# Kernel optimization log

Hardware: AMD Instinct MI355X
Metric: run time of the kernel (lower is better)

Reference implementation:

```python
import jax, jax.numpy as jnp
import numpy as np


def _demosaic_kernels():
    kgrb = 1/8 * np.array([[0,0,-1,0,0],[0,0,2,0,0],[-1,2,4,2,-1],[0,0,2,0,0],[0,0,-1,0,0]], dtype=np.float32)
    krbg0 = 1/8 * np.array([[0,0,0.5,0,0],[0,-1,0,-1,0],[-1,4,5,4,-1],[0,-1,0,-1,0],[0,0,0.5,0,0]], dtype=np.float32)
    krbg1 = krbg0.T
    krbbr = 1/8 * np.array([[0,0,-1.5,0,0],[0,2,0,2,0],[-1.5,0,6,0,-1.5],[0,2,0,2,0],[0,0,-1.5,0,0]], dtype=np.float32)
    return jnp.asarray(np.stack([kgrb, krbg0, krbg1, krbbr], 0)[:, None, :, :])  # (4,1,5,5)


def setup_inputs() -> dict:
    key = jax.random.key(0)
    x = jax.random.uniform(key, (4, 1, 2048, 2048), dtype=jnp.float32)  # RGGB bayer mosaic
    k = _demosaic_kernels()
    return {"x": x, "k": k}


def reference(x, k):
    # reflect-pad by 2 on H and W, then fixed 4-filter 5x5 conv
    xp = jnp.pad(x, ((0, 0), (0, 0), (2, 2), (2, 2)), mode="reflect")
    cfa = jax.lax.conv_general_dilated(
        xp, k, window_strides=(1, 1), padding="VALID",
        dimension_numbers=("NCHW", "OIHW", "NCHW"))  # (N,4,H,W)
    out = jnp.tile(x, (1, 3, 1, 1))  # (N,3,H,W)
    # green at R and B sites
    out = out.at[:, 1, 0::2, 0::2].set(cfa[:, 0, 0::2, 0::2])
    out = out.at[:, 1, 1::2, 1::2].set(cfa[:, 0, 1::2, 1::2])
    # red at G/B sites
    out = out.at[:, 0, 0::2, 1::2].set(cfa[:, 1, 0::2, 1::2])
    out = out.at[:, 0, 1::2, 0::2].set(cfa[:, 2, 1::2, 0::2])
    out = out.at[:, 0, 1::2, 1::2].set(cfa[:, 3, 1::2, 1::2])
    # blue at G/R sites
    out = out.at[:, 2, 0::2, 1::2].set(cfa[:, 2, 0::2, 1::2])
    out = out.at[:, 2, 1::2, 0::2].set(cfa[:, 1, 1::2, 0::2])
    out = out.at[:, 2, 0::2, 0::2].set(cfa[:, 3, 0::2, 0::2])
    return jnp.clip(out, 0.0, 1.0)
```

## Files before the change

kernel.cpp:

```cpp
#include <hip/hip_runtime.h>

#define IMG_H 2048
#define IMG_W 2048
#define NIMG 4

__device__ __forceinline__ int refl(int i, int n) {
    i = (i < 0) ? -i : i;
    return (i >= n) ? (2 * n - 2 - i) : i;
}

__device__ __forceinline__ float clamp01(float v) {
    return fminf(fmaxf(v, 0.0f), 1.0f);
}

__device__ __forceinline__ void px_rgb(
    float x0,
    float xl, float xr, float xll, float xrr,
    float xu, float xd, float xuu, float xdd,
    float dul, float dur, float ddl, float ddr,
    int pr, int pc,
    float& R, float& G, float& B)
{
    float h1 = xl + xr, v1 = xu + xd;
    float h2 = xll + xrr, v2 = xuu + xdd;
    float diag = dul + dur + ddl + ddr;
    float cfa0 = 0.125f * (4.0f * x0 + 2.0f * (h1 + v1) - (h2 + v2));
    float cfa1 = 0.125f * (5.0f * x0 + 4.0f * h1 - h2 + 0.5f * v2 - diag);
    float cfa2 = 0.125f * (5.0f * x0 + 4.0f * v1 - v2 + 0.5f * h2 - diag);
    float cfa3 = 0.125f * (6.0f * x0 + 2.0f * diag - 1.5f * (h2 + v2));

    if (pr == 0) {
        if (pc == 0) { R = x0;   G = cfa0; B = cfa3; }
        else         { R = cfa1; G = x0;   B = cfa2; }
    } else {
        if (pc == 0) { R = cfa2; G = x0;   B = cfa1; }
        else         { R = cfa3; G = cfa0; B = x0;   }
    }
    R = clamp01(R); G = clamp01(G); B = clamp01(B);
}

__global__ __launch_bounds__(256) void demosaic_kernel(
    const float* __restrict__ x, float* __restrict__ out)
{
    const int QW = IMG_W / 4;
    int idx = blockIdx.x * blockDim.x + threadIdx.x;
    int c4   = idx & (QW - 1);
    int rest = idx >> 9;
    int r = rest & (IMG_H - 1);
    int n = rest >> 11;
    int c = c4 * 4;

    const float* p = x + (size_t)n * IMG_H * IMG_W;
    int pr = r & 1;
    float R[4], G[4], B[4];

    bool interior = (r >= 2) && (r <= IMG_H - 3) && (c >= 4) && (c <= IMG_W - 8);
    if (interior) {
        const float* pm2 = p + (size_t)(r - 2) * IMG_W + c;
        const float* pm1 = p + (size_t)(r - 1) * IMG_W + c;
        const float* p0  = p + (size_t)(r    ) * IMG_W + c;
        const float* pp1 = p + (size_t)(r + 1) * IMG_W + c;
        const float* pp2 = p + (size_t)(r + 2) * IMG_W + c;

        float w0[8], wm1[6], wp1[6], wm2[4], wp2[4];
        #pragma unroll
        for (int i = 0; i < 8; i++) w0[i] = p0[i - 2];
        #pragma unroll
        for (int i = 0; i < 6; i++) { wm1[i] = pm1[i - 1]; wp1[i] = pp1[i - 1]; }
        #pragma unroll
        for (int i = 0; i < 4; i++) { wm2[i] = pm2[i]; wp2[i] = pp2[i]; }

        #pragma unroll
        for (int j = 0; j < 4; j++) {
            px_rgb(w0[j + 2],
                   w0[j + 1], w0[j + 3], w0[j], w0[j + 4],
                   wm1[j + 1], wp1[j + 1], wm2[j], wp2[j],
                   wm1[j], wm1[j + 2], wp1[j], wp1[j + 2],
                   pr, j & 1,
                   R[j], G[j], B[j]);
        }
    } else {
        int rm1 = refl(r - 1, IMG_H), rm2 = refl(r - 2, IMG_H);
        int rp1 = refl(r + 1, IMG_H), rp2 = refl(r + 2, IMG_H);
        const float* p0r  = p + (size_t)r   * IMG_W;
        const float* pm1r = p + (size_t)rm1 * IMG_W;
        const float* pm2r = p + (size_t)rm2 * IMG_W;
        const float* pp1r = p + (size_t)rp1 * IMG_W;
        const float* pp2r = p + (size_t)rp2 * IMG_W;
        #pragma unroll
        for (int j = 0; j < 4; j++) {
            int cc  = c + j;
            int cm1 = refl(cc - 1, IMG_W), cm2 = refl(cc - 2, IMG_W);
            int cp1 = refl(cc + 1, IMG_W), cp2 = refl(cc + 2, IMG_W);
            px_rgb(p0r[cc],
                   p0r[cm1], p0r[cp1], p0r[cm2], p0r[cp2],
                   pm1r[cc], pp1r[cc], pm2r[cc], pp2r[cc],
                   pm1r[cm1], pm1r[cp1], pp1r[cm1], pp1r[cp1],
                   pr, cc & 1,
                   R[j], G[j], B[j]);
        }
    }

    const size_t plane = (size_t)IMG_H * IMG_W;
    size_t ob = (size_t)n * 3 * plane + (size_t)r * IMG_W + c;
    *(float4*)(out + ob)             = make_float4(R[0], R[1], R[2], R[3]);
    *(float4*)(out + ob + plane)     = make_float4(G[0], G[1], G[2], G[3]);
    *(float4*)(out + ob + 2 * plane) = make_float4(B[0], B[1], B[2], B[3]);
}

extern "C" void kernel_launch(void* const* d_in, const int* in_sizes, int n_in,
                              void* d_out, int out_size, void* d_ws, size_t ws_size,
                              hipStream_t stream) {
    const float* x = (const float*)d_in[0];
    float* out = (float*)d_out;
    const int total = NIMG * IMG_H * (IMG_W / 4);
    dim3 block(256);
    dim3 grid(total / 256);
    demosaic_kernel<<<grid, block, 0, stream>>>(x, out);
}
```

Before: 272.9 us.

## Process two rows per thread with aligned float4 neighborhood loads

Each thread now computes a 2x4 pixel block covering both Bayer row parities instead of a 1x4 strip, and the grid is halved to match. The 6-row stencil window is fetched as aligned float4 loads and shared between the two output rows, which cuts redundant neighbor reads and removes runtime parity branching. The cost is more registers per thread and half as many threads in flight. The kernel is memory-bound, so the gain depends mostly on fewer load instructions, since cache traffic was already mostly reused.

```diff
diff --git a/kernel.cpp b/kernel.cpp
--- a/kernel.cpp
+++ b/kernel.cpp
@@ -42,70 +42,93 @@
 __global__ __launch_bounds__(256) void demosaic_kernel(
     const float* __restrict__ x, float* __restrict__ out)
 {
-    const int QW = IMG_W / 4;
     int idx = blockIdx.x * blockDim.x + threadIdx.x;
-    int c4   = idx & (QW - 1);
+    int c4   = idx & 511;
     int rest = idx >> 9;
-    int r = rest & (IMG_H - 1);
-    int n = rest >> 11;
-    int c = c4 * 4;
+    int rp   = rest & 1023;
+    int n    = rest >> 10;
+    int r = rp << 1;
+    int c = c4 << 2;
 
     const float* p = x + (size_t)n * IMG_H * IMG_W;
-    int pr = r & 1;
-    float R[4], G[4], B[4];
+    const size_t plane = (size_t)IMG_H * IMG_W;
+    size_t ob = (size_t)n * 3 * plane + (size_t)r * IMG_W + c;
 
-    bool interior = (r >= 2) && (r <= IMG_H - 3) && (c >= 4) && (c <= IMG_W - 8);
+    bool interior = (r >= 2) && (r <= IMG_H - 4) && (c >= 4) && (c <= IMG_W - 8);
     if (interior) {
-        const float* pm2 = p + (size_t)(r - 2) * IMG_W + c;
-        const float* pm1 = p + (size_t)(r - 1) * IMG_W + c;
-        const float* p0  = p + (size_t)(r    ) * IMG_W + c;
-        const float* pp1 = p + (size_t)(r + 1) * IMG_W + c;
-        const float* pp2 = p + (size_t)(r + 2) * IMG_W + c;
+        const float* b = p + (size_t)r * IMG_W + c;
+        float4 m2  = *(const float4*)(b - 2 * IMG_W);
+        float4 m1l = *(const float4*)(b - IMG_W - 4);
+        float4 m1c = *(const float4*)(b - IMG_W);
+        float4 m1r = *(const float4*)(b - IMG_W + 4);
+        float4 z0l = *(const float4*)(b - 4);
+        float4 z0c = *(const float4*)(b);
+        float4 z0r = *(const float4*)(b + 4);
+        float4 z1l = *(const float4*)(b + IMG_W - 4);
+        float4 z1c = *(const float4*)(b + IMG_W);
+        float4 z1r = *(const float4*)(b + IMG_W + 4);
+        float4 z2l = *(const float4*)(b + 2 * IMG_W - 4);
+        float4 z2c = *(const float4*)(b + 2 * IMG_W);
+        float4 z2r = *(const float4*)(b + 2 * IMG_W + 4);
+        float4 p3  = *(const float4*)(b + 3 * IMG_W);
 
-        float w0[8], wm1[6], wp1[6], wm2[4], wp2[4];
-        #pragma unroll
-        for (int i = 0; i < 8; i++) w0[i] = p0[i - 2];
-        #pragma unroll
-        for (int i = 0; i < 6; i++) { wm1[i] = pm1[i - 1]; wp1[i] = pp1[i - 1]; }
-        #pragma unroll
-        for (int i = 0; i < 4; i++) { wm2[i] = pm2[i]; wp2[i] = pp2[i]; }
+        float wm2[4] = {m2.x, m2.y, m2.z, m2.w};
+        float wm1[6] = {m1l.w, m1c.x, m1c.y, m1c.z, m1c.w, m1r.x};
+        float w0[8]  = {z0l.z, z0l.w, z0c.x, z0c.y, z0c.z, z0c.w, z0r.x, z0r.y};
+        float w1[8]  = {z1l.z, z1l.w, z1c.x, z1c.y, z1c.z, z1c.w, z1r.x, z1r.y};
+        float w2[6]  = {z2l.w, z2c.x, z2c.y, z2c.z, z2c.w, z2r.x};
+        float w3[4]  = {p3.x, p3.y, p3.z, p3.w};
 
+        float R0[4], G0[4], B0[4], R1[4], G1[4], B1[4];
         #pragma unroll
         for (int j = 0; j < 4; j++) {
             px_rgb(w0[j + 2],
                    w0[j + 1], w0[j + 3], w0[j], w0[j + 4],
-                   wm1[j + 1], wp1[j + 1], wm2[j], wp2[j],
-                   wm1[j], wm1[j + 2], wp1[j], wp1[j + 2],
-                   pr, j & 1,
-                   R[j], G[j], B[j]);
+                   wm1[j + 1], w1[j + 2], wm2[j], w2[j + 1],
+                   wm1[j], wm1[j + 2], w1[j + 1], w1[j + 3],
+                   0, j & 1, R0[j], G0[j], B0[j]);
+            px_rgb(w1[j + 2],
+                   w1[j + 1], w1[j + 3], w1[j], w1[j + 4],
+                   w0[j + 2], w2[j + 1], wm1[j + 1], w3[j],
+                   w0[j + 1], w0[j + 3], w2[j], w2[j + 2],
+                   1, j & 1, R1[j], G1[j], B1[j]);
         }
+
+        *(float4*)(out + ob)                     = make_float4(R0[0], R0[1], R0[2], R0[3]);
+        *(float4*)(out + ob + plane)             = make_float4(G0[0], G0[1], G0[2], G0[3]);
+        *(float4*)(out + ob + 2 * plane)         = make_float4(B0[0], B0[1], B0[2], B0[3]);
+        *(float4*)(out + ob + IMG_W)             = make_float4(R1[0], R1[1], R1[2], R1[3]);
+        *(float4*)(out + ob + IMG_W + plane)     = make_float4(G1[0], G1[1], G1[2], G1[3]);
+        *(float4*)(out + ob + IMG_W + 2 * plane) = make_float4(B1[0], B1[1], B1[2], B1[3]);
     } else {
-        int rm1 = refl(r - 1, IMG_H), rm2 = refl(r - 2, IMG_H);
-        int rp1 = refl(r + 1, IMG_H), rp2 = refl(r + 2, IMG_H);
-        const float* p0r  = p + (size_t)r   * IMG_W;
-        const float* pm1r = p + (size_t)rm1 * IMG_W;
-        const float* pm2r = p + (size_t)rm2 * IMG_W;
-        const float* pp1r = p + (size_t)rp1 * IMG_W;
-        const float* pp2r = p + (size_t)rp2 * IMG_W;
         #pragma unroll
-        for (int j = 0; j < 4; j++) {
-            int cc  = c + j;
-            int cm1 = refl(cc - 1, IMG_W), cm2 = refl(cc - 2, IMG_W);
-            int cp1 = refl(cc + 1, IMG_W), cp2 = refl(cc + 2, IMG_W);
-            px_rgb(p0r[cc],
-                   p0r[cm1], p0r[cp1], p0r[cm2], p0r[cp2],
-                   pm1r[cc], pp1r[cc], pm2r[cc], pp2r[cc],
-                   pm1r[cm1], pm1r[cp1], pp1r[cm1], pp1r[cp1],
-                   pr, cc & 1,
-                   R[j], G[j], B[j]);
+        for (int i = 0; i < 2; i++) {
+            int rr = r + i;
+            int rm1 = refl(rr - 1, IMG_H), rm2 = refl(rr - 2, IMG_H);
+            int rp1 = refl(rr + 1, IMG_H), rp2 = refl(rr + 2, IMG_H);
+            const float* p0r  = p + (size_t)rr  * IMG_W;
+            const float* pm1r = p + (size_t)rm1 * IMG_W;
+            const float* pm2r = p + (size_t)rm2 * IMG_W;
+            const float* pp1r = p + (size_t)rp1 * IMG_W;
+            const float* pp2r = p + (size_t)rp2 * IMG_W;
+            #pragma unroll
+            for (int j = 0; j < 4; j++) {
+                int cc  = c + j;
+                int cm1 = refl(cc - 1, IMG_W), cm2 = refl(cc - 2, IMG_W);
+                int cp1 = refl(cc + 1, IMG_W), cp2 = refl(cc + 2, IMG_W);
+                float R, G, B;
+                px_rgb(p0r[cc],
+                       p0r[cm1], p0r[cp1], p0r[cm2], p0r[cp2],
+                       pm1r[cc], pp1r[cc], pm2r[cc], pp2r[cc],
+                       pm1r[cm1], pm1r[cp1], pp1r[cm1], pp1r[cp1],
+                       i, cc & 1, R, G, B);
+                size_t o = ob + (size_t)i * IMG_W + j;
+                out[o]             = R;
+                out[o + plane]     = G;
+                out[o + 2 * plane] = B;
+            }
         }
     }
-
-    const size_t plane = (size_t)IMG_H * IMG_W;
-    size_t ob = (size_t)n * 3 * plane + (size_t)r * IMG_W + c;
-    *(float4*)(out + ob)             = make_float4(R[0], R[1], R[2], R[3]);
-    *(float4*)(out + ob + plane)     = make_float4(G[0], G[1], G[2], G[3]);
-    *(float4*)(out + ob + 2 * plane) = make_float4(B[0], B[1], B[2], B[3]);
 }
 
 extern "C" void kernel_launch(void* const* d_in, const int* in_sizes, int n_in,
@@ -113,7 +136,7 @@
                               hipStream_t stream) {
     const float* x = (const float*)d_in[0];
     float* out = (float*)d_out;
-    const int total = NIMG * IMG_H * (IMG_W / 4);
+    const int total = NIMG * (IMG_H / 2) * (IMG_W / 4);
     dim3 block(256);
     dim3 grid(total / 256);
     demosaic_kernel<<<grid, block, 0, stream>>>(x, out);
```

Result: faster. 266.4 us (-2.4%).
